# Kernel tuning notes

Measured on AMD Instinct MI355X. Metric: run time of the kernel, lower is better.

## Reference

```python
import jax, jax.numpy as jnp
import numpy as np

B, Q, KV = 2, 2048, 2048
D_MODEL = 1024
N_HEADS = 16
D_KV = 64
EPS = 1e-6


def setup_inputs() -> dict:
    key = jax.random.key(0)
    ks = jax.random.split(key, 7)
    s = 0.02
    return {
        "hidden_states": jax.random.normal(ks[0], (B, Q, D_MODEL), jnp.float32),
        "key_value_states": jax.random.normal(ks[1], (B, KV, D_MODEL), jnp.float32),
        "wq": jax.random.normal(ks[2], (D_MODEL, N_HEADS * D_KV), jnp.float32) * s,
        "wk": jax.random.normal(ks[3], (D_MODEL, N_HEADS * D_KV), jnp.float32) * s,
        "wv": jax.random.normal(ks[4], (D_MODEL, N_HEADS * D_KV), jnp.float32) * s,
        "wo": jax.random.normal(ks[5], (N_HEADS * D_KV, D_MODEL), jnp.float32) * s,
        "norm_w": jnp.ones((D_MODEL,), jnp.float32),
    }


def reference(hidden_states, key_value_states, wq, wk, wv, wo, norm_w):
    # RMSNorm (T5-style, no mean subtraction)
    var = jnp.mean(jnp.square(hidden_states), axis=-1, keepdims=True)
    normed = hidden_states * jax.lax.rsqrt(var + EPS) * norm_w

    b, q_len, _ = hidden_states.shape
    kv_len = key_value_states.shape[1]

    def split_heads(x):  # [b, s, H*d] -> [b, H, s, d]
        return x.reshape(b, -1, N_HEADS, D_KV).transpose(0, 2, 1, 3)

    q = split_heads(normed @ wq)              # [b,H,q,d]
    k = split_heads(key_value_states @ wk)    # [b,H,kv,d]
    v = split_heads(key_value_states @ wv)    # [b,H,kv,d]

    # T5 attention: NO 1/sqrt(d) scaling; position_bias is zeros here
    # (has_relative_attention_bias=False, no mask) so it is a no-op.
    scores = jnp.einsum("bhqd,bhkd->bhqk", q, k)
    attn = jax.nn.softmax(scores.astype(jnp.float32), axis=-1).astype(scores.dtype)
    ctx = jnp.einsum("bhqk,bhkd->bhqd", attn, v)
    ctx = ctx.transpose(0, 2, 1, 3).reshape(b, q_len, N_HEADS * D_KV)
    attn_out = ctx @ wo

    # residual connection
    return hidden_states + attn_out
```

## Files before the change

### kernel.cpp

```cpp
#include <hip/hip_runtime.h>


typedef __attribute__((ext_vector_type(8))) short  s16x8;
typedef __attribute__((ext_vector_type(4))) float  f32x4;
typedef __attribute__((ext_vector_type(4))) int    i32x4;

#define LOG2E 1.4426950408889634f
#define EXP2(x) __builtin_amdgcn_exp2f(x)

__device__ __forceinline__ unsigned short f2bf(float f) {
  unsigned int u = __builtin_bit_cast(unsigned int, f);
  return (unsigned short)((u + 0x7FFFu + ((u >> 16) & 1u)) >> 16);
}

__device__ __forceinline__ unsigned cvtpk(float lo, float hi) {
  unsigned r;
  asm("v_cvt_pk_bf16_f32 %0, %1, %2" : "=v"(r) : "v"(lo), "v"(hi));
  return r;
}

__device__ __forceinline__ void gload16(const void* g, void* l) {
  __builtin_amdgcn_global_load_lds(
      (const __attribute__((address_space(1))) unsigned int*)g,
      (__attribute__((address_space(3))) unsigned int*)l, 16, 0, 0);
}

__global__ __launch_bounds__(256) void k_transpose4(
    const float* __restrict__ a0, const float* __restrict__ a1,
    const float* __restrict__ a2, const float* __restrict__ a3,
    unsigned short* __restrict__ o0, unsigned short* __restrict__ o1,
    unsigned short* __restrict__ o2, unsigned short* __restrict__ o3) {
  int z = blockIdx.z;
  const float* in = (z == 0) ? a0 : (z == 1) ? a1 : (z == 2) ? a2 : a3;
  unsigned short* out = (z == 0) ? o0 : (z == 1) ? o1 : (z == 2) ? o2 : o3;
  __shared__ float tile[64][65];
  int t = threadIdx.x;
  int tx = t & 15, ty = t >> 4;
  int r0 = blockIdx.y * 64, c0 = blockIdx.x * 64;
#pragma unroll
  for (int p = 0; p < 4; ++p) {
    int r = p * 16 + ty;
    float4 v = *reinterpret_cast<const float4*>(in + (size_t)(r0 + r) * 1024 + c0 + tx * 4);
    tile[r][tx * 4 + 0] = v.x; tile[r][tx * 4 + 1] = v.y;
    tile[r][tx * 4 + 2] = v.z; tile[r][tx * 4 + 3] = v.w;
  }
  __syncthreads();
#pragma unroll
  for (int p = 0; p < 4; ++p) {
    int c = p * 16 + ty;
    unsigned int lo = (unsigned int)f2bf(tile[tx * 4 + 0][c]) |
                      ((unsigned int)f2bf(tile[tx * 4 + 1][c]) << 16);
    unsigned int hi = (unsigned int)f2bf(tile[tx * 4 + 2][c]) |
                      ((unsigned int)f2bf(tile[tx * 4 + 3][c]) << 16);
    uint2 pk2; pk2.x = lo; pk2.y = hi;
    *reinterpret_cast<uint2*>(out + (size_t)(c0 + c) * 1024 + r0 + tx * 4) = pk2;
  }
}

__global__ __launch_bounds__(256) void k_rmsnorm(
    const float* __restrict__ hs, const float* __restrict__ w,
    unsigned short* __restrict__ out) {
  int row = blockIdx.x, t = threadIdx.x;
  float4 v = *reinterpret_cast<const float4*>(hs + (size_t)row * 1024 + t * 4);
  float s = v.x * v.x + v.y * v.y + v.z * v.z + v.w * v.w;
#pragma unroll
  for (int m = 1; m < 64; m <<= 1) s += __shfl_xor(s, m);
  __shared__ float ps[4];
  if ((t & 63) == 0) ps[t >> 6] = s;
  __syncthreads();
  float tot = ps[0] + ps[1] + ps[2] + ps[3];
  float sc = rsqrtf(tot * (1.0f / 1024.0f) + 1e-6f) * LOG2E;
  float4 wv = *reinterpret_cast<const float4*>(w + t * 4);
  unsigned int lo = (unsigned int)f2bf(v.x * sc * wv.x) |
                    ((unsigned int)f2bf(v.y * sc * wv.y) << 16);
  unsigned int hi = (unsigned int)f2bf(v.z * sc * wv.z) |
                    ((unsigned int)f2bf(v.w * sc * wv.w) << 16);
  uint2 pk2; pk2.x = lo; pk2.y = hi;
  *reinterpret_cast<uint2*>(out + (size_t)row * 1024 + t * 4) = pk2;
}

__global__ __launch_bounds__(256) void k_cast(
    const float* __restrict__ in, unsigned short* __restrict__ out, int n4) {
  int i = blockIdx.x * 256 + threadIdx.x;
  int stride = gridDim.x * 256;
  for (; i < n4; i += stride) {
    float4 v = *reinterpret_cast<const float4*>(in + (size_t)i * 4);
    unsigned int lo = (unsigned int)f2bf(v.x) | ((unsigned int)f2bf(v.y) << 16);
    unsigned int hi = (unsigned int)f2bf(v.z) | ((unsigned int)f2bf(v.w) << 16);
    uint2 pk2; pk2.x = lo; pk2.y = hi;
    *reinterpret_cast<uint2*>(out + (size_t)i * 4) = pk2;
  }
}

__device__ __forceinline__ void gemm_body(
    const unsigned short* __restrict__ A, const unsigned short* __restrict__ Bt,
    void* __restrict__ Cout, const float* __restrict__ resid, int mode) {
  __shared__ __align__(16) char sm[65536];
  int t = threadIdx.x;
  int bn = blockIdx.x, bm = blockIdx.y;
  int m0 = bm * 128, n0 = bn * 128;
  int lane = t & 63, w = t >> 6, lr = lane & 15, lg = lane >> 4;
  int wr = w >> 1, wc = w & 1;

  f32x4 acc[4][4] = {};

  const char* aA = (const char*)A + ((size_t)(m0 + (t >> 3)) * 1024 + (t & 7) * 8) * 2;
  const char* aB = (const char*)Bt + ((size_t)(n0 + (t >> 3)) * 1024 + (t & 7) * 8) * 2;

  auto stage = [&](int buf, int kt) {
    int koff = kt * 128;
    char* As = sm + buf * 16384;
    char* Bs = sm + 32768 + buf * 16384;
#pragma unroll
    for (int c = 0; c < 4; ++c) {
      gload16(aA + (size_t)c * 65536 + koff, As + c * 4096 + t * 16);
      gload16(aB + (size_t)c * 65536 + koff, Bs + c * 4096 + t * 16);
    }
  };

  stage(0, 0);
  __syncthreads();
  int cur = 0;
  for (int kt = 0; kt < 16; ++kt) {
    if (kt < 15) stage(cur ^ 1, kt + 1);
    const char* As = sm + cur * 16384;
    const char* Bs = sm + 32768 + cur * 16384;
    s16x8 af[2][4], bfr[2][4];
#pragma unroll
    for (int ks = 0; ks < 2; ++ks) {
#pragma unroll
      for (int m = 0; m < 4; ++m)
        af[ks][m] = *reinterpret_cast<const s16x8*>(
            As + (wr * 64 + m * 16 + lr) * 128 + ks * 64 + lg * 16);
#pragma unroll
      for (int n = 0; n < 4; ++n)
        bfr[ks][n] = *reinterpret_cast<const s16x8*>(
            Bs + (wc * 64 + n * 16 + lr) * 128 + ks * 64 + lg * 16);
    }
#pragma unroll
    for (int ks = 0; ks < 2; ++ks)
#pragma unroll
      for (int m = 0; m < 4; ++m)
#pragma unroll
        for (int n = 0; n < 4; ++n)
          acc[m][n] = __builtin_amdgcn_mfma_f32_16x16x32_bf16(af[ks][m], bfr[ks][n], acc[m][n], 0, 0, 0);
    __syncthreads();
    cur ^= 1;
  }

#pragma unroll
  for (int m = 0; m < 4; ++m)
#pragma unroll
    for (int n = 0; n < 4; ++n) {
      int colg = n0 + wc * 64 + n * 16 + lr;
      int rowb = m0 + wr * 64 + m * 16 + lg * 4;
      if (mode == 0) {
        unsigned short* C = (unsigned short*)Cout;
#pragma unroll
        for (int r = 0; r < 4; ++r)
          C[(size_t)(rowb + r) * 1024 + colg] = f2bf(acc[m][n][r]);
      } else if (mode == 1) {
        int h = colg >> 6, d = colg & 63;
        int b = rowb >> 11, kv = rowb & 2047;
        unsigned short* C = (unsigned short*)Cout +
            ((size_t)((b * 16 + h) * 64 + d) * 2048 + kv);
        unsigned int lo = (unsigned int)f2bf(acc[m][n][0]) |
                          ((unsigned int)f2bf(acc[m][n][1]) << 16);
        unsigned int hi = (unsigned int)f2bf(acc[m][n][2]) |
                          ((unsigned int)f2bf(acc[m][n][3]) << 16);
        uint2 pk2; pk2.x = lo; pk2.y = hi;
        *reinterpret_cast<uint2*>(C) = pk2;
      } else {
        float* C = (float*)Cout;
#pragma unroll
        for (int r = 0; r < 4; ++r) {
          size_t idx = (size_t)(rowb + r) * 1024 + colg;
          C[idx] = resid[idx] + acc[m][n][r];
        }
      }
    }
}

__global__ __launch_bounds__(256) void k_gemm_qkv(
    const unsigned short* __restrict__ normed, const unsigned short* __restrict__ kvb,
    const unsigned short* __restrict__ wqT, const unsigned short* __restrict__ wkT,
    const unsigned short* __restrict__ wvT,
    unsigned short* __restrict__ qb, unsigned short* __restrict__ kb,
    unsigned short* __restrict__ vTb) {
  int z = blockIdx.z;
  const unsigned short* A = (z == 0) ? normed : kvb;
  const unsigned short* B = (z == 0) ? wqT : (z == 1) ? wkT : wvT;
  void* C = (z == 0) ? (void*)qb : (z == 1) ? (void*)kb : (void*)vTb;
  gemm_body(A, B, C, nullptr, (z == 2) ? 1 : 0);
}

__global__ __launch_bounds__(256) void k_gemm_o(
    const unsigned short* __restrict__ ctxb, const unsigned short* __restrict__ woT,
    float* __restrict__ out, const float* __restrict__ hs) {
  gemm_body(ctxb, woT, (void*)out, hs, 2);
}

__global__ __launch_bounds__(256) void k_attn(
    const unsigned short* __restrict__ q, const unsigned short* __restrict__ k,
    const unsigned short* __restrict__ vt, unsigned short* __restrict__ ctx) {
  __shared__ __align__(16) char sm[65536];
  int t = threadIdx.x, w = t >> 6, lane = t & 63, lr = lane & 15, lg = lane >> 4;

  int bid = blockIdx.x;
  int xcd = bid & 7, slot = bid >> 3;
  int bh = xcd * 4 + (slot >> 4);
  int qt = slot & 15;
  int b = bh >> 4, h = bh & 15;

  const char* qB = (const char*)q + ((size_t)(b * 2048 + qt * 128) * 1024 + h * 64) * 2;
  const char* kB = (const char*)k + ((size_t)(b * 2048) * 1024 + h * 64) * 2;
  const char* vB = (const char*)vt + (size_t)bh * 64 * 4096;

  int krow = t >> 3;
  int kcb  = ((t & 7) * 16) ^ ((krow & 7) << 4);
  int vrow = t >> 4;
  int vcb  = ((t & 15) * 16) ^ ((vrow & 7) << 4);

  auto stageKV = [&](int buf, int it2) {
    char* Kd = sm + buf * 16384;
    char* Vd = sm + 32768 + buf * 16384;
    const char* kb2 = kB + (size_t)(it2 * 128) * 2048;
    const char* vb2 = vB + it2 * 256;
#pragma unroll
    for (int c = 0; c < 4; ++c) {
      gload16(kb2 + (size_t)(c * 32 + krow) * 2048 + kcb, Kd + c * 4096 + t * 16);
      gload16(vb2 + (size_t)(c * 16 + vrow) * 4096 + vcb, Vd + c * 4096 + t * 16);
    }
  };

#pragma unroll
  for (int c = 0; c < 4; ++c)
    gload16(qB + (size_t)(c * 32 + krow) * 2048 + kcb, sm + c * 4096 + t * 16);
  __syncthreads();
  s16x8 qa[2][2];
#pragma unroll
  for (int mm = 0; mm < 2; ++mm)
#pragma unroll
    for (int ks = 0; ks < 2; ++ks) {
      int row = w * 32 + mm * 16 + lr;
      qa[mm][ks] = *reinterpret_cast<const s16x8*>(
          sm + row * 128 + ((ks * 64 + lg * 16) ^ ((lr & 7) << 4)));
    }
  __syncthreads();
  stageKV(0, 0);
  asm volatile("s_waitcnt vmcnt(0)" ::: "memory");
  __builtin_amdgcn_s_barrier();
  __builtin_amdgcn_sched_barrier(0);

  f32x4 octx[2][4] = {};
  float mrun[2] = {-1e30f, -1e30f};
  float lsum[2] = {0.0f, 0.0f};

  int cur = 0;
  for (int it = 0; it < 16; ++it) {
    if (it < 15) stageKV(cur ^ 1, it + 1);

    const char* Ks = sm + cur * 16384;
    const char* Vs = sm + 32768 + cur * 16384;

    f32x4 s2[2][8] = {};
#pragma unroll
    for (int ks = 0; ks < 2; ++ks) {
      s16x8 ka[8];
#pragma unroll
      for (int n = 0; n < 8; ++n)
        ka[n] = *reinterpret_cast<const s16x8*>(
            Ks + (n * 16 + lr) * 128 + ((ks * 64 + lg * 16) ^ ((lr & 7) << 4)));
#pragma unroll
      for (int mm = 0; mm < 2; ++mm)
#pragma unroll
        for (int n = 0; n < 8; ++n)
          s2[mm][n] = __builtin_amdgcn_mfma_f32_16x16x32_bf16(ka[n], qa[mm][ks], s2[mm][n], 0, 0, 0);
    }

    float m2[2];
#pragma unroll
    for (int mm = 0; mm < 2; ++mm) {
      float v = s2[mm][0][0];
#pragma unroll
      for (int n = 0; n < 8; ++n)
#pragma unroll
        for (int r = 0; r < 4; ++r) v = fmaxf(v, s2[mm][n][r]);
      v = fmaxf(v, __shfl_xor(v, 16));
      v = fmaxf(v, __shfl_xor(v, 32));
      m2[mm] = v;
    }
    int need = (m2[0] > mrun[0] + 8.0f) || (m2[1] > mrun[1] + 8.0f);
    if (__any(need)) {
#pragma unroll
      for (int mm = 0; mm < 2; ++mm) {
        float mx = fmaxf(mrun[mm], m2[mm]);
        float sc = EXP2(mrun[mm] - mx);
        mrun[mm] = mx;
        lsum[mm] *= sc;
#pragma unroll
        for (int r = 0; r < 4; ++r) {
          float scr = __shfl(sc, lg * 4 + r);
#pragma unroll
          for (int nd = 0; nd < 4; ++nd) octx[mm][nd][r] *= scr;
        }
      }
    }

    unsigned pk[2][8][2];
#pragma unroll
    for (int mm = 0; mm < 2; ++mm) {
      float a0 = 0.0f, a1 = 0.0f, a2 = 0.0f, a3 = 0.0f;
#pragma unroll
      for (int n = 0; n < 8; ++n) {
        float p0 = EXP2(s2[mm][n][0] - mrun[mm]);
        float p1 = EXP2(s2[mm][n][1] - mrun[mm]);
        float p2 = EXP2(s2[mm][n][2] - mrun[mm]);
        float p3 = EXP2(s2[mm][n][3] - mrun[mm]);
        a0 += p0; a1 += p1; a2 += p2; a3 += p3;
        pk[mm][n][0] = cvtpk(p0, p1);
        pk[mm][n][1] = cvtpk(p2, p3);
      }
      lsum[mm] += (a0 + a1) + (a2 + a3);
    }

#pragma unroll
    for (int ks = 0; ks < 4; ++ks) {
      s16x8 vb[4];
#pragma unroll
      for (int nd = 0; nd < 4; ++nd) {
        int row = nd * 16 + lr;
        int swz = (lr & 7) << 4;
        uint2 v1 = *reinterpret_cast<const uint2*>(
            Vs + row * 256 + ((ks * 64 + lg * 8) ^ swz));
        uint2 v2 = *reinterpret_cast<const uint2*>(
            Vs + row * 256 + ((ks * 64 + 32 + lg * 8) ^ swz));
        i32x4 vv; vv[0] = (int)v1.x; vv[1] = (int)v1.y;
        vv[2] = (int)v2.x; vv[3] = (int)v2.y;
        vb[nd] = __builtin_bit_cast(s16x8, vv);
      }
#pragma unroll
      for (int mm = 0; mm < 2; ++mm) {
        i32x4 pv;
        pv[0] = (int)pk[mm][2 * ks][0];     pv[1] = (int)pk[mm][2 * ks][1];
        pv[2] = (int)pk[mm][2 * ks + 1][0]; pv[3] = (int)pk[mm][2 * ks + 1][1];
        s16x8 pa = __builtin_bit_cast(s16x8, pv);
#pragma unroll
        for (int nd = 0; nd < 4; ++nd)
          octx[mm][nd] = __builtin_amdgcn_mfma_f32_16x16x32_bf16(pa, vb[nd], octx[mm][nd], 0, 0, 0);
      }
    }

    if (it < 15) {
      asm volatile("s_waitcnt vmcnt(0)" ::: "memory");
      __builtin_amdgcn_s_barrier();
      __builtin_amdgcn_sched_barrier(0);
      cur ^= 1;
    }
  }

#pragma unroll
  for (int mm = 0; mm < 2; ++mm) {
    float tot = lsum[mm];
    tot += __shfl_xor(tot, 16);
    tot += __shfl_xor(tot, 32);
    float inv = 1.0f / tot;
#pragma unroll
    for (int r = 0; r < 4; ++r) {
      float invr = __shfl(inv, lg * 4 + r);
      int qrow = qt * 128 + w * 32 + mm * 16 + lg * 4 + r;
#pragma unroll
      for (int nd = 0; nd < 4; ++nd)
        ctx[(size_t)(b * 2048 + qrow) * 1024 + h * 64 + nd * 16 + lr] =
            f2bf(octx[mm][nd][r] * invr);
    }
  }
}

extern "C" void kernel_launch(void* const* d_in, const int* in_sizes, int n_in,
                              void* d_out, int out_size, void* d_ws, size_t ws_size,
                              hipStream_t stream) {
  const float* hs  = (const float*)d_in[0];
  const float* kvs = (const float*)d_in[1];
  const float* wq  = (const float*)d_in[2];
  const float* wk  = (const float*)d_in[3];
  const float* wv  = (const float*)d_in[4];
  const float* wo  = (const float*)d_in[5];
  const float* nw  = (const float*)d_in[6];
  float* out = (float*)d_out;
  char* ws = (char*)d_ws;

  unsigned short* normed = (unsigned short*)(ws + (size_t)0);
  unsigned short* kvb    = (unsigned short*)(ws + ((size_t)8 << 20));
  unsigned short* wqT    = (unsigned short*)(ws + ((size_t)16 << 20));
  unsigned short* wkT    = (unsigned short*)(ws + ((size_t)18 << 20));
  unsigned short* wvT    = (unsigned short*)(ws + ((size_t)20 << 20));
  unsigned short* woT    = (unsigned short*)(ws + ((size_t)22 << 20));
  unsigned short* qb     = (unsigned short*)(ws + ((size_t)24 << 20));
  unsigned short* kb     = (unsigned short*)(ws + ((size_t)32 << 20));
  unsigned short* vTb    = (unsigned short*)(ws + ((size_t)40 << 20));
  unsigned short* ctxb   = (unsigned short*)(ws + ((size_t)48 << 20));

  k_transpose4<<<dim3(16, 16, 4), 256, 0, stream>>>(wq, wk, wv, wo, wqT, wkT, wvT, woT);
  k_rmsnorm<<<4096, 256, 0, stream>>>(hs, nw, normed);
  k_cast<<<1024, 256, 0, stream>>>(kvs, kvb, 1048576);

  k_gemm_qkv<<<dim3(8, 32, 3), 256, 0, stream>>>(normed, kvb, wqT, wkT, wvT, qb, kb, vTb);

  k_attn<<<512, 256, 0, stream>>>(qb, kb, vTb, ctxb);

  k_gemm_o<<<dim3(8, 32), 256, 0, stream>>>(ctxb, woT, out, hs);
}
```

Baseline: 140.7 us.

## Halve LDS tiles in GEMMs and attention to raise occupancy

The GEMM body becomes a template over row-tile height and output mode. Its K step drops from 128 to 64 and its LDS shrinks accordingly, and the output projection now uses 64-row tiles over twice as many blocks. The attention kernel streams 64-key tiles instead of 128, which cuts its LDS from 64KB to 32KB, and all kernels gain launch_bounds(256,4) so more workgroups can sit on each CU. The aim is better latency hiding through occupancy, at the cost of twice as many barriers and loop iterations, shorter MFMA runs between syncs, and a tighter register budget that could cause spills.

```diff
diff --git a/kernel.cpp b/kernel.cpp
--- a/kernel.cpp
+++ b/kernel.cpp
@@ -92,74 +92,74 @@
   }
 }
 
+template <int BM, int MODE>
 __device__ __forceinline__ void gemm_body(
     const unsigned short* __restrict__ A, const unsigned short* __restrict__ Bt,
-    void* __restrict__ Cout, const float* __restrict__ resid, int mode) {
-  __shared__ __align__(16) char sm[65536];
+    void* __restrict__ Cout, const float* __restrict__ resid) {
+  constexpr int MF = BM / 32;
+  constexpr int ATILE = BM * 64;
+  __shared__ __align__(16) char sm[2 * ATILE + 16384];
   int t = threadIdx.x;
   int bn = blockIdx.x, bm = blockIdx.y;
-  int m0 = bm * 128, n0 = bn * 128;
+  int m0 = bm * BM, n0 = bn * 128;
   int lane = t & 63, w = t >> 6, lr = lane & 15, lg = lane >> 4;
   int wr = w >> 1, wc = w & 1;
 
-  f32x4 acc[4][4] = {};
-
-  const char* aA = (const char*)A + ((size_t)(m0 + (t >> 3)) * 1024 + (t & 7) * 8) * 2;
-  const char* aB = (const char*)Bt + ((size_t)(n0 + (t >> 3)) * 1024 + (t & 7) * 8) * 2;
+  f32x4 acc[MF][4] = {};
+
+  const char* aA = (const char*)A + ((size_t)(m0 + (t >> 2)) * 1024 + (t & 3) * 8) * 2;
+  const char* aB = (const char*)Bt + ((size_t)(n0 + (t >> 2)) * 1024 + (t & 3) * 8) * 2;
 
   auto stage = [&](int buf, int kt) {
-    int koff = kt * 128;
-    char* As = sm + buf * 16384;
-    char* Bs = sm + 32768 + buf * 16384;
-#pragma unroll
-    for (int c = 0; c < 4; ++c) {
-      gload16(aA + (size_t)c * 65536 + koff, As + c * 4096 + t * 16);
-      gload16(aB + (size_t)c * 65536 + koff, Bs + c * 4096 + t * 16);
-    }
+    int koff = kt * 64;
+    char* As = sm + buf * ATILE;
+    char* Bs = sm + 2 * ATILE + buf * 8192;
+#pragma unroll
+    for (int c = 0; c < BM / 64; ++c)
+      gload16(aA + (size_t)c * 131072 + koff, As + c * 4096 + t * 16);
+#pragma unroll
+    for (int c = 0; c < 2; ++c)
+      gload16(aB + (size_t)c * 131072 + koff, Bs + c * 4096 + t * 16);
   };
 
   stage(0, 0);
   __syncthreads();
   int cur = 0;
-  for (int kt = 0; kt < 16; ++kt) {
-    if (kt < 15) stage(cur ^ 1, kt + 1);
-    const char* As = sm + cur * 16384;
-    const char* Bs = sm + 32768 + cur * 16384;
-    s16x8 af[2][4], bfr[2][4];
-#pragma unroll
-    for (int ks = 0; ks < 2; ++ks) {
-#pragma unroll
-      for (int m = 0; m < 4; ++m)
-        af[ks][m] = *reinterpret_cast<const s16x8*>(
-            As + (wr * 64 + m * 16 + lr) * 128 + ks * 64 + lg * 16);
+  for (int kt = 0; kt < 32; ++kt) {
+    if (kt < 31) stage(cur ^ 1, kt + 1);
+    const char* As = sm + cur * ATILE;
+    const char* Bs = sm + 2 * ATILE + cur * 8192;
+    s16x8 af[MF], bfr[4];
+#pragma unroll
+    for (int m = 0; m < MF; ++m)
+      af[m] = *reinterpret_cast<const s16x8*>(
+          As + (wr * (BM / 2) + m * 16 + lr) * 64 + lg * 16);
+#pragma unroll
+    for (int n = 0; n < 4; ++n)
+      bfr[n] = *reinterpret_cast<const s16x8*>(
+          Bs + (wc * 64 + n * 16 + lr) * 64 + lg * 16);
+#pragma unroll
+    for (int m = 0; m < MF; ++m)
 #pragma unroll
       for (int n = 0; n < 4; ++n)
-        bfr[ks][n] = *reinterpret_cast<const s16x8*>(
-            Bs + (wc * 64 + n * 16 + lr) * 128 + ks * 64 + lg * 16);
-    }
-#pragma unroll
-    for (int ks = 0; ks < 2; ++ks)
-#pragma unroll
-      for (int m = 0; m < 4; ++m)
-#pragma unroll
-        for (int n = 0; n < 4; ++n)
-          acc[m][n] = __builtin_amdgcn_mfma_f32_16x16x32_bf16(af[ks][m], bfr[ks][n], acc[m][n], 0, 0, 0);
-    __syncthreads();
+        acc[m][n] = __builtin_amdgcn_mfma_f32_16x16x32_bf16(af[m], bfr[n], acc[m][n], 0, 0, 0);
+    asm volatile("s_waitcnt vmcnt(0)" ::: "memory");
+    __builtin_amdgcn_s_barrier();
     cur ^= 1;
   }
 
 #pragma unroll
-  for (int m = 0; m < 4; ++m)
+  for (int m = 0; m < MF; ++m)
 #pragma unroll
     for (int n = 0; n < 4; ++n) {
       int colg = n0 + wc * 64 + n * 16 + lr;
-      int rowb = m0 + wr * 64 + m * 16 + lg * 4;
-      if (mode == 0) {
+      int rowb = m0 + wr * (BM / 2) + m * 16 + lg * 4;
+      if (MODE == 0) {
         unsigned short* C = (unsigned short*)Cout;
 #pragma unroll
         for (int r = 0; r < 4; ++r)
           C[(size_t)(rowb + r) * 1024 + colg] = f2bf(acc[m][n][r]);
-      } else if (mode == 1) {
+      } else if (MODE == 1) {
         int h = colg >> 6, d = colg & 63;
         int b = rowb >> 11, kv = rowb & 2047;
         unsigned short* C = (unsigned short*)Cout +
@@ -181,7 +181,7 @@
     }
 }
 
-__global__ __launch_bounds__(256) void k_gemm_qkv(
+__global__ __launch_bounds__(256, 4) void k_gemm_qkv(
     const unsigned short* __restrict__ normed, const unsigned short* __restrict__ kvb,
     const unsigned short* __restrict__ wqT, const unsigned short* __restrict__ wkT,
     const unsigned short* __restrict__ wvT,
@@ -190,20 +190,24 @@
   int z = blockIdx.z;
   const unsigned short* A = (z == 0) ? normed : kvb;
   const unsigned short* B = (z == 0) ? wqT : (z == 1) ? wkT : wvT;
-  void* C = (z == 0) ? (void*)qb : (z == 1) ? (void*)kb : (void*)vTb;
-  gemm_body(A, B, C, nullptr, (z == 2) ? 1 : 0);
-}
-
-__global__ __launch_bounds__(256) void k_gemm_o(
+  if (z == 2)
+    gemm_body<128, 1>(A, B, (void*)vTb, nullptr);
+  else if (z == 1)
+    gemm_body<128, 0>(A, B, (void*)kb, nullptr);
+  else
+    gemm_body<128, 0>(A, B, (void*)qb, nullptr);
+}
+
+__global__ __launch_bounds__(256, 4) void k_gemm_o(
     const unsigned short* __restrict__ ctxb, const unsigned short* __restrict__ woT,
     float* __restrict__ out, const float* __restrict__ hs) {
-  gemm_body(ctxb, woT, (void*)out, hs, 2);
-}
-
-__global__ __launch_bounds__(256) void k_attn(
+  gemm_body<64, 2>(ctxb, woT, (void*)out, hs);
+}
+
+__global__ __launch_bounds__(256, 4) void k_attn(
     const unsigned short* __restrict__ q, const unsigned short* __restrict__ k,
     const unsigned short* __restrict__ vt, unsigned short* __restrict__ ctx) {
-  __shared__ __align__(16) char sm[65536];
+  __shared__ __align__(16) char sm[32768];
   int t = threadIdx.x, w = t >> 6, lane = t & 63, lr = lane & 15, lg = lane >> 4;
 
   int bid = blockIdx.x;
@@ -216,26 +220,24 @@
   const char* kB = (const char*)k + ((size_t)(b * 2048) * 1024 + h * 64) * 2;
   const char* vB = (const char*)vt + (size_t)bh * 64 * 4096;
 
-  int krow = t >> 3;
-  int kcb  = ((t & 7) * 16) ^ ((krow & 7) << 4);
-  int vrow = t >> 4;
-  int vcb  = ((t & 15) * 16) ^ ((vrow & 7) << 4);
+  int srow = t >> 3;
+  int scb  = ((t & 7) * 16) ^ ((srow & 7) << 4);
 
   auto stageKV = [&](int buf, int it2) {
-    char* Kd = sm + buf * 16384;
-    char* Vd = sm + 32768 + buf * 16384;
-    const char* kb2 = kB + (size_t)(it2 * 128) * 2048;
-    const char* vb2 = vB + it2 * 256;
-#pragma unroll
-    for (int c = 0; c < 4; ++c) {
-      gload16(kb2 + (size_t)(c * 32 + krow) * 2048 + kcb, Kd + c * 4096 + t * 16);
-      gload16(vb2 + (size_t)(c * 16 + vrow) * 4096 + vcb, Vd + c * 4096 + t * 16);
+    char* Kd = sm + buf * 8192;
+    char* Vd = sm + 16384 + buf * 8192;
+    const char* kb2 = kB + (size_t)(it2 * 64) * 2048;
+    const char* vb2 = vB + it2 * 128;
+#pragma unroll
+    for (int c = 0; c < 2; ++c) {
+      gload16(kb2 + (size_t)(c * 32 + srow) * 2048 + scb, Kd + c * 4096 + t * 16);
+      gload16(vb2 + (size_t)(c * 32 + srow) * 4096 + scb, Vd + c * 4096 + t * 16);
     }
   };
 
 #pragma unroll
   for (int c = 0; c < 4; ++c)
-    gload16(qB + (size_t)(c * 32 + krow) * 2048 + kcb, sm + c * 4096 + t * 16);
+    gload16(qB + (size_t)(c * 32 + srow) * 2048 + scb, sm + c * 4096 + t * 16);
   __syncthreads();
   s16x8 qa[2][2];
 #pragma unroll
@@ -257,24 +259,24 @@
   float lsum[2] = {0.0f, 0.0f};
 
   int cur = 0;
-  for (int it = 0; it < 16; ++it) {
-    if (it < 15) stageKV(cur ^ 1, it + 1);
-
-    const char* Ks = sm + cur * 16384;
-    const char* Vs = sm + 32768 + cur * 16384;
-
-    f32x4 s2[2][8] = {};
+  for (int it = 0; it < 32; ++it) {
+    if (it < 31) stageKV(cur ^ 1, it + 1);
+
+    const char* Ks = sm + cur * 8192;
+    const char* Vs = sm + 16384 + cur * 8192;
+
+    f32x4 s2[2][4] = {};
 #pragma unroll
     for (int ks = 0; ks < 2; ++ks) {
-      s16x8 ka[8];
-#pragma unroll
-      for (int n = 0; n < 8; ++n)
+      s16x8 ka[4];
+#pragma unroll
+      for (int n = 0; n < 4; ++n)
         ka[n] = *reinterpret_cast<const s16x8*>(
             Ks + (n * 16 + lr) * 128 + ((ks * 64 + lg * 16) ^ ((lr & 7) << 4)));
 #pragma unroll
       for (int mm = 0; mm < 2; ++mm)
 #pragma unroll
-        for (int n = 0; n < 8; ++n)
+        for (int n = 0; n < 4; ++n)
           s2[mm][n] = __builtin_amdgcn_mfma_f32_16x16x32_bf16(ka[n], qa[mm][ks], s2[mm][n], 0, 0, 0);
     }
 
@@ -283,7 +285,7 @@
     for (int mm = 0; mm < 2; ++mm) {
       float v = s2[mm][0][0];
 #pragma unroll
-      for (int n = 0; n < 8; ++n)
+      for (int n = 0; n < 4; ++n)
 #pragma unroll
         for (int r = 0; r < 4; ++r) v = fmaxf(v, s2[mm][n][r]);
       v = fmaxf(v, __shfl_xor(v, 16));
@@ -307,12 +309,12 @@
       }
     }
 
-    unsigned pk[2][8][2];
+    unsigned pk[2][4][2];
 #pragma unroll
     for (int mm = 0; mm < 2; ++mm) {
       float a0 = 0.0f, a1 = 0.0f, a2 = 0.0f, a3 = 0.0f;
 #pragma unroll
-      for (int n = 0; n < 8; ++n) {
+      for (int n = 0; n < 4; ++n) {
         float p0 = EXP2(s2[mm][n][0] - mrun[mm]);
         float p1 = EXP2(s2[mm][n][1] - mrun[mm]);
         float p2 = EXP2(s2[mm][n][2] - mrun[mm]);
@@ -325,16 +327,16 @@
     }
 
 #pragma unroll
-    for (int ks = 0; ks < 4; ++ks) {
+    for (int ks = 0; ks < 2; ++ks) {
       s16x8 vb[4];
 #pragma unroll
       for (int nd = 0; nd < 4; ++nd) {
         int row = nd * 16 + lr;
         int swz = (lr & 7) << 4;
         uint2 v1 = *reinterpret_cast<const uint2*>(
-            Vs + row * 256 + ((ks * 64 + lg * 8) ^ swz));
+            Vs + row * 128 + ((ks * 64 + lg * 8) ^ swz));
         uint2 v2 = *reinterpret_cast<const uint2*>(
-            Vs + row * 256 + ((ks * 64 + 32 + lg * 8) ^ swz));
+            Vs + row * 128 + ((ks * 64 + 32 + lg * 8) ^ swz));
         i32x4 vv; vv[0] = (int)v1.x; vv[1] = (int)v1.y;
         vv[2] = (int)v2.x; vv[3] = (int)v2.y;
         vb[nd] = __builtin_bit_cast(s16x8, vv);
@@ -351,7 +353,7 @@
       }
     }
 
-    if (it < 15) {
+    if (it < 31) {
       asm volatile("s_waitcnt vmcnt(0)" ::: "memory");
       __builtin_amdgcn_s_barrier();
       __builtin_amdgcn_sched_barrier(0);
@@ -409,5 +411,5 @@
 
   k_attn<<<512, 256, 0, stream>>>(qb, kb, vTb, ctxb);
 
-  k_gemm_o<<<dim3(8, 32), 256, 0, stream>>>(ctxb, woT, out, hs);
-}
+  k_gemm_o<<<dim3(8, 64), 256, 0, stream>>>(ctxb, woT, out, hs);
+}
```

Result: slower. 164.6 us (+17.0%).
